# Kernel optimization log

Measured on AMD Instinct MI355X. Metric: run time of the kernel, lower is better.

## Reference

```python
import jax, jax.numpy as jnp
import numpy as np

N = 384       # nodes
K = 60        # neighbors per node
SUB = 20      # subsample_k
C_S = 128
C_Z = 128
H = 4
D_HEAD = C_Z // H
NUM_RBF = 64
E = N * K
EPS = 1e-8


def _rbf(D, D_min=0.0, D_max=20.0, D_count=NUM_RBF):
    # radial basis expansion of distances: [..., ] -> [..., D_count]
    mu = jnp.linspace(D_min, D_max, D_count)
    sigma = (D_max - D_min) / D_count
    return jnp.exp(-(((D[..., None] - mu) / sigma) ** 2))


def setup_inputs() -> dict:
    key = jax.random.key(0)
    ks = jax.random.split(key, 16)
    f32 = jnp.float32
    inp = {
        "node_features": jax.random.normal(ks[0], (N, C_S), f32),
        "node_trans": jax.random.normal(ks[1], (N, 3), f32) * 5.0,
        "edge_features": jax.random.normal(ks[2], (E, C_Z), f32),
        "edge_index": jax.random.randint(ks[3], (2, E), 0, N),
        "subsample_idx": jax.random.randint(ks[4], (N, K, SUB), 0, K),
        # dist_bias_gate: Linear(2*c_s -> H)
        "W_gate": jax.random.normal(ks[5], (2 * C_S, H), f32) / np.sqrt(2 * C_S),
        "b_gate": jnp.zeros((H,), f32),
        # dist_bias: Linear(num_rbf -> H)
        "W_db": jax.random.normal(ks[6], (NUM_RBF, H), f32) / np.sqrt(NUM_RBF),
        "b_db": jnp.zeros((H,), f32),
        # lin_qk: Linear(c_z -> 2*c_z)
        "W_qk": jax.random.normal(ks[7], (C_Z, 2 * C_Z), f32) / np.sqrt(C_Z),
        "b_qk": jnp.zeros((2 * C_Z,), f32),
        # lin_v: Linear(c_z -> c_z)
        "W_v": jax.random.normal(ks[8], (C_Z, C_Z), f32) / np.sqrt(C_Z),
        "b_v": jnp.zeros((C_Z,), f32),
        # lin_out: Linear(c_z -> c_z) (init='final' in source; random here for testing)
        "W_out": jax.random.normal(ks[9], (C_Z, C_Z), f32) / np.sqrt(C_Z),
        "b_out": jnp.zeros((C_Z,), f32),
    }
    return inp


def reference(node_features, node_trans, edge_features, edge_index, subsample_idx,
              W_gate, b_gate, W_db, b_db, W_qk, b_qk, W_v, b_v, W_out, b_out):
    n, k, sub = subsample_idx.shape
    # assume_sorted=True path: edges are grouped k-per-destination-node
    dst = edge_index[0].reshape(n, k)                           # [n,k] neighbor ids
    edge1 = jnp.broadcast_to(dst[:, :, None], (n, k, sub))      # [n,k,sub]
    edge2 = jnp.take_along_axis(
        jnp.broadcast_to(dst[:, None, :], (n, k, k)), subsample_idx, axis=-1)  # [n,k,sub]

    f1 = node_features[edge1]                                   # [n,k,sub,c_s]
    f2 = node_features[edge2]
    gate = jax.nn.sigmoid(jnp.concatenate([f1, f2], axis=-1) @ W_gate + b_gate)  # [n,k,sub,H]

    t1 = node_trans[edge1]                                      # [n,k,sub,3]
    t2 = node_trans[edge2]
    dist = jnp.linalg.norm(t1 - t2 + EPS, axis=-1)              # [n,k,sub]
    bias = gate * (_rbf(dist) @ W_db + b_db)                    # [n,k,sub,H]

    edges = edge_features.reshape(n, k, C_Z)
    qk = edges @ W_qk + b_qk
    q, kk = jnp.split(qk, 2, axis=-1)
    q = q.reshape(n, k, H, D_HEAD)
    kk = kk.reshape(n, k, H, D_HEAD)

    batch = jnp.arange(n)[:, None, None]
    k_sub = kk[batch, subsample_idx]                            # [n,k,sub,H,d]
    attn = jnp.einsum('nkhd,nkshd->nksh', q, k_sub) / np.sqrt(C_Z) + bias
    attn = jax.nn.softmax(attn, axis=2)                         # softmax over subsample axis

    v = (edges @ W_v + b_v).reshape(n, k, H, D_HEAD)
    v_sub = v[batch, subsample_idx]                             # [n,k,sub,H,d]
    upd = jnp.einsum('nksh,nkshd->nkhd', attn, v_sub).reshape(n * k, C_Z)
    return upd @ W_out + b_out                                  # [E, c_z]
```

## Files before the change

kernel.cpp:

```cpp
#include <hip/hip_runtime.h>
#include <hip/hip_bf16.h>

typedef unsigned short ushortT;
typedef __attribute__((ext_vector_type(8))) short bf16x8;
typedef __attribute__((ext_vector_type(4))) float f32x4;

#define N_NODES 384
#define KNBR 60
#define SUBK 20
#define NEDGE (N_NODES * KNBR)
#define EPSC 1e-8f
#define INV_SQRT_CZ 0.08838834764831845f
#define MU_STEP (20.0f / 63.0f)
#define INV_MU_STEP (63.0f / 20.0f)
#define INV_SIGMA 3.2f

__device__ __forceinline__ float bflo(unsigned int u) { return __uint_as_float(u << 16); }
__device__ __forceinline__ float bfhi(unsigned int u) { return __uint_as_float(u & 0xffff0000u); }
__device__ __forceinline__ ushortT f2bu(float v) {
  union { float f; unsigned int u; } c;
  c.f = v;
  return (ushortT)((c.u + 0x7fffu + ((c.u >> 16) & 1u)) >> 16);
}
__device__ __forceinline__ unsigned int pack2bf(float x, float y) {
  return (unsigned int)f2bu(x) | ((unsigned int)f2bu(y) << 16);
}
__device__ __forceinline__ ushortT f2h(float x) {
  _Float16 h = (_Float16)x;
  return __builtin_bit_cast(ushortT, h);
}
__device__ __forceinline__ float h2f(ushortT u) {
  return (float)__builtin_bit_cast(_Float16, u);
}

__global__ __launch_bounds__(256) void prep_kernel(
    const float* __restrict__ nf, const float* __restrict__ Wg, float* __restrict__ g,
    const float* __restrict__ Wqk, const float* __restrict__ bqk,
    const float* __restrict__ Wv, const float* __restrict__ bv,
    const float* __restrict__ Wout,
    ushortT* __restrict__ Wp1, ushortT* __restrict__ Wp2, float* __restrict__ bc) {
  int b = blockIdx.x, tid = threadIdx.x;
  if (b < 96) {
    int n = b * 4 + (tid >> 6), t = tid & 63;
    float a = nf[n * 128 + t];
    float bb = nf[n * 128 + 64 + t];
    float acc[8];
#pragma unroll
    for (int h = 0; h < 4; ++h) {
      acc[h]     = a * Wg[t * 4 + h]         + bb * Wg[(t + 64) * 4 + h];
      acc[4 + h] = a * Wg[(128 + t) * 4 + h] + bb * Wg[(192 + t) * 4 + h];
    }
#pragma unroll
    for (int i = 0; i < 8; ++i)
#pragma unroll
      for (int off = 32; off >= 1; off >>= 1) acc[i] += __shfl_xor(acc[i], off, 64);
    if (t == 0) {
#pragma unroll
      for (int i = 0; i < 8; ++i) g[n * 8 + i] = acc[i];
    }
  } else {
    int i = (b - 96) * 256 + tid;
    if (i < 49152) {
      int j = i & 7, l = (i >> 3) & 63, t = (i >> 9) & 3;
      int nt = (i >> 11) % 12, ny = (i >> 11) / 12;
      int nn = ny * 192 + nt * 16 + (l & 15);
      int k = t * 32 + (l >> 4) * 8 + j;
      float v = (nn < 256) ? Wqk[k * 256 + nn] : Wv[k * 128 + (nn - 256)];
      Wp1[i] = f2bu(v);
    } else {
      int i2 = i - 49152;
      int j = i2 & 7, l = (i2 >> 3) & 63, t = (i2 >> 9) & 3, nt = (i2 >> 11);
      int nn = nt * 16 + (l & 15);
      int k = t * 32 + (l >> 4) * 8 + j;
      Wp2[i2] = f2bu(Wout[k * 128 + nn]);
    }
    if (i < 384) bc[i] = (i < 256) ? bqk[i] : bv[i - 256];
  }
}

__global__ __launch_bounds__(512, 4) void fused_kernel(
    const float* __restrict__ ef, const ushortT* __restrict__ Wp1,
    const ushortT* __restrict__ Wp2, const float* __restrict__ bc,
    const float* __restrict__ bout, const float* __restrict__ g,
    const float* __restrict__ node_trans, const int* __restrict__ edge_index,
    const int* __restrict__ sub_idx, const float* __restrict__ W_db,
    const float* __restrict__ b_db, const float* __restrict__ b_gate,
    float* __restrict__ outp) {
  __shared__ __align__(16) ushortT kvb[KNBR * 256];
  __shared__ __align__(16) ushortT updq[64 * 136];
  __shared__ __align__(16) ushortT biasb[KNBR * SUBK * 4];
  __shared__ ushortT sub_lds[KNBR * SUBK];
  __shared__ float trs[KNBR * 3];
  __shared__ float gg[KNBR * 8];

  int n = blockIdx.x, tid = threadIdx.x;
  int e0 = n * KNBR;
  int w = tid >> 6, l = tid & 63;
  int lr = l & 15, lc = l >> 4;
  int rowA = (w & 3) * 16 + lr;
  int rowAc = min(rowA, KNBR - 1);

  if (tid < KNBR) {
    int dst = edge_index[e0 + tid];
#pragma unroll
    for (int c = 0; c < 3; ++c) trs[tid * 3 + c] = node_trans[dst * 3 + c];
#pragma unroll
    for (int i = 0; i < 8; ++i) gg[tid * 8 + i] = g[dst * 8 + i];
  }
  bf16x8 afrag[4];
#pragma unroll
  for (int t = 0; t < 4; ++t) {
    const float* ap = ef + (size_t)(e0 + rowAc) * 128 + t * 32 + lc * 8;
    float4 lo = *(const float4*)ap;
    float4 hi = *(const float4*)(ap + 4);
    bf16x8 a;
    a[0] = (short)f2bu(lo.x); a[1] = (short)f2bu(lo.y);
    a[2] = (short)f2bu(lo.z); a[3] = (short)f2bu(lo.w);
    a[4] = (short)f2bu(hi.x); a[5] = (short)f2bu(hi.y);
    a[6] = (short)f2bu(hi.z); a[7] = (short)f2bu(hi.w);
    afrag[t] = a;
  }

  int Tbase = (tid >> 8) * 12;
#pragma unroll
  for (int Ti = 0; Ti < 12; ++Ti) {
    int T = Tbase + Ti;
    f32x4 acc = {0.f, 0.f, 0.f, 0.f};
#pragma unroll
    for (int t = 0; t < 4; ++t) {
      bf16x8 bfrag = *(const bf16x8*)(Wp1 + ((T * 4 + t) * 64 + l) * 8);
      acc = __builtin_amdgcn_mfma_f32_16x16x32_bf16(bfrag, afrag[t], acc, 0, 0, 0);
    }
    int col0 = T * 16 + lc * 4;
    float4 bi = *(const float4*)(bc + col0);
    float o0 = acc[0] + bi.x, o1 = acc[1] + bi.y;
    float o2 = acc[2] + bi.z, o3 = acc[3] + bi.w;
    if (T < 8) {
      uint2 o;
      o.x = pack2bf(o0 * INV_SQRT_CZ, o1 * INV_SQRT_CZ);
      o.y = pack2bf(o2 * INV_SQRT_CZ, o3 * INV_SQRT_CZ);
      *(uint2*)(updq + rowA * 136 + col0) = o;
    } else if (rowA < KNBR) {
      uint2 o;
      o.x = pack2bf(o0, o1);
      o.y = pack2bf(o2, o3);
      int byteoff = ((col0 - 128) * 2) ^ ((rowA & 7) << 4);
      *(uint2*)((char*)kvb + rowA * 512 + byteoff) = o;
    }
  }
  __syncthreads();

  float4 bgv = *(const float4*)b_gate;
  float4 bdbv = *(const float4*)b_db;
  for (int p = tid; p < KNBR * SUBK; p += 512) {
    int kl = p / SUBK, s = p - kl * SUBK;
    int j = sub_idx[(size_t)(e0 + kl) * SUBK + s];
    sub_lds[p] = (ushortT)j;
    float dx = trs[kl * 3 + 0] - trs[j * 3 + 0] + EPSC;
    float dy = trs[kl * 3 + 1] - trs[j * 3 + 1] + EPSC;
    float dz = trs[kl * 3 + 2] - trs[j * 3 + 2] + EPSC;
    float dist = sqrtf(dx * dx + dy * dy + dz * dz);
    int r0 = (int)(dist * INV_MU_STEP + 0.5f);
    int rlo = max(r0 - 4, 0), rhi = min(r0 + 4, 63);
    float a0 = 0.f, a1 = 0.f, a2 = 0.f, a3 = 0.f;
    for (int r = rlo; r <= rhi; ++r) {
      float t = (dist - r * MU_STEP) * INV_SIGMA;
      float e = __expf(-t * t);
      float4 wv = ((const float4*)W_db)[r];
      a0 += e * wv.x; a1 += e * wv.y; a2 += e * wv.z; a3 += e * wv.w;
    }
    float g1 = gg[kl * 8 + 0] + gg[j * 8 + 4 + 0] + bgv.x;
    float g2 = gg[kl * 8 + 1] + gg[j * 8 + 4 + 1] + bgv.y;
    float g3 = gg[kl * 8 + 2] + gg[j * 8 + 4 + 2] + bgv.z;
    float g4 = gg[kl * 8 + 3] + gg[j * 8 + 4 + 3] + bgv.w;
    biasb[p * 4 + 0] = f2h((a0 + bdbv.x) / (1.0f + __expf(-g1)));
    biasb[p * 4 + 1] = f2h((a1 + bdbv.y) / (1.0f + __expf(-g2)));
    biasb[p * 4 + 2] = f2h((a2 + bdbv.z) / (1.0f + __expf(-g3)));
    biasb[p * 4 + 3] = f2h((a3 + bdbv.w) / (1.0f + __expf(-g4)));
  }
  __syncthreads();

  int row3 = tid >> 3, h = (tid >> 1) & 3, dh = tid & 1;
  int row3c = min(row3, KNBR - 1);
  const char* kvbase = (const char*)kvb;
  float qh[16];
  {
    const ushortT* qp = updq + row3 * 136 + h * 32 + dh * 16;
    uint4 u0 = *(const uint4*)qp;
    uint4 u1 = *(const uint4*)(qp + 8);
    qh[0] = bflo(u0.x); qh[1] = bfhi(u0.x); qh[2] = bflo(u0.y); qh[3] = bfhi(u0.y);
    qh[4] = bflo(u0.z); qh[5] = bfhi(u0.z); qh[6] = bflo(u0.w); qh[7] = bfhi(u0.w);
    qh[8] = bflo(u1.x); qh[9] = bfhi(u1.x); qh[10] = bflo(u1.y); qh[11] = bfhi(u1.y);
    qh[12] = bflo(u1.z); qh[13] = bfhi(u1.z); qh[14] = bflo(u1.w); qh[15] = bfhi(u1.w);
  }
  float logit[SUBK];
#pragma unroll
  for (int s = 0; s < SUBK; ++s) {
    int j = sub_lds[row3c * SUBK + s];
    int sw = (j & 7) << 4;
    float dot = 0.f;
#pragma unroll
    for (int c = 0; c < 2; ++c) {
      uint4 u = *(const uint4*)(kvbase + j * 512 + ((h * 64 + dh * 32 + c * 16) ^ sw));
      dot += qh[c * 8 + 0] * bflo(u.x) + qh[c * 8 + 1] * bfhi(u.x) +
             qh[c * 8 + 2] * bflo(u.y) + qh[c * 8 + 3] * bfhi(u.y) +
             qh[c * 8 + 4] * bflo(u.z) + qh[c * 8 + 5] * bfhi(u.z) +
             qh[c * 8 + 6] * bflo(u.w) + qh[c * 8 + 7] * bfhi(u.w);
    }
    dot += __shfl_xor(dot, 1);
    logit[s] = dot + h2f(biasb[(row3c * SUBK + s) * 4 + h]);
  }
  float m = logit[0];
#pragma unroll
  for (int s = 1; s < SUBK; ++s) m = fmaxf(m, logit[s]);
  float den = 0.f;
#pragma unroll
  for (int s = 0; s < SUBK; ++s) {
    logit[s] = __expf(logit[s] - m);
    den += logit[s];
  }
  float inv = 1.0f / den;
  float vacc[16];
#pragma unroll
  for (int i = 0; i < 16; ++i) vacc[i] = 0.f;
#pragma unroll
  for (int s = 0; s < SUBK; ++s) {
    int j = sub_lds[row3c * SUBK + s];
    int sw = (j & 7) << 4;
    float wgt = logit[s];
#pragma unroll
    for (int c = 0; c < 2; ++c) {
      uint4 u = *(const uint4*)(kvbase + j * 512 + ((256 + h * 64 + dh * 32 + c * 16) ^ sw));
      vacc[c * 8 + 0] += wgt * bflo(u.x); vacc[c * 8 + 1] += wgt * bfhi(u.x);
      vacc[c * 8 + 2] += wgt * bflo(u.y); vacc[c * 8 + 3] += wgt * bfhi(u.y);
      vacc[c * 8 + 4] += wgt * bflo(u.z); vacc[c * 8 + 5] += wgt * bfhi(u.z);
      vacc[c * 8 + 6] += wgt * bflo(u.w); vacc[c * 8 + 7] += wgt * bfhi(u.w);
    }
  }
#pragma unroll
  for (int c = 0; c < 2; ++c) {
    uint4 o;
    o.x = pack2bf(vacc[c * 8 + 0] * inv, vacc[c * 8 + 1] * inv);
    o.y = pack2bf(vacc[c * 8 + 2] * inv, vacc[c * 8 + 3] * inv);
    o.z = pack2bf(vacc[c * 8 + 4] * inv, vacc[c * 8 + 5] * inv);
    o.w = pack2bf(vacc[c * 8 + 6] * inv, vacc[c * 8 + 7] * inv);
    *(uint4*)(updq + row3 * 136 + h * 32 + dh * 16 + c * 8) = o;
  }
  __syncthreads();

  bf16x8 af2[4];
#pragma unroll
  for (int t = 0; t < 4; ++t)
    af2[t] = *(const bf16x8*)(updq + rowA * 136 + t * 32 + lc * 8);
  int T4base = (tid >> 8) * 4;
#pragma unroll
  for (int Ti = 0; Ti < 4; ++Ti) {
    int T = T4base + Ti;
    f32x4 acc = {0.f, 0.f, 0.f, 0.f};
#pragma unroll
    for (int t = 0; t < 4; ++t) {
      bf16x8 bfrag = *(const bf16x8*)(Wp2 + ((T * 4 + t) * 64 + l) * 8);
      acc = __builtin_amdgcn_mfma_f32_16x16x32_bf16(bfrag, af2[t], acc, 0, 0, 0);
    }
    if (rowA < KNBR) {
      int col0 = T * 16 + lc * 4;
      float4 bi = *(const float4*)(bout + col0);
      float4 o;
      o.x = acc[0] + bi.x; o.y = acc[1] + bi.y;
      o.z = acc[2] + bi.z; o.w = acc[3] + bi.w;
      *(float4*)(outp + (size_t)(e0 + rowA) * 128 + col0) = o;
    }
  }
}

extern "C" void kernel_launch(void* const* d_in, const int* in_sizes, int n_in, void* d_out,
                              int out_size, void* d_ws, size_t ws_size, hipStream_t stream) {
  const float* nf  = (const float*)d_in[0];
  const float* nt  = (const float*)d_in[1];
  const float* ef  = (const float*)d_in[2];
  const int*   ei  = (const int*)d_in[3];
  const int*   si  = (const int*)d_in[4];
  const float* Wg  = (const float*)d_in[5];
  const float* bg  = (const float*)d_in[6];
  const float* Wdb = (const float*)d_in[7];
  const float* bdb = (const float*)d_in[8];
  const float* Wqk = (const float*)d_in[9];
  const float* bqk = (const float*)d_in[10];
  const float* Wv  = (const float*)d_in[11];
  const float* bv  = (const float*)d_in[12];
  const float* Wout = (const float*)d_in[13];
  const float* bout = (const float*)d_in[14];
  float* out = (float*)d_out;

  float* g      = (float*)d_ws;
  float* bc     = g + 3072;
  ushortT* Wp1  = (ushortT*)(bc + 384);
  ushortT* Wp2  = Wp1 + 49152;

  prep_kernel<<<dim3(352), dim3(256), 0, stream>>>(nf, Wg, g, Wqk, bqk, Wv, bv, Wout,
                                                   Wp1, Wp2, bc);
  fused_kernel<<<dim3(N_NODES), dim3(512), 0, stream>>>(ef, Wp1, Wp2, bc, bout, g, nt, ei, si,
                                                        Wdb, bdb, bg, out);
}
```

Measured before the change: 40.20 us.

## Split each node's edge rows across two 256-thread blocks

Launches a 384x2 grid of 256-thread blocks, each handling 30 of the 60 edge rows for Q, bias, attention and output. Every block still computes the full K/V projection for all 60 neighbours, since subsampled keys can come from either half. The K/V LDS layout is also re-swizzled so each thread's head slice sits in 16-byte chunks. The aim is more blocks and better CU fill, at the cost of doing the K/V GEMM and the ef loads twice.

```diff
diff --git a/kernel.cpp b/kernel.cpp
--- a/kernel.cpp
+++ b/kernel.cpp
@@ -14,6 +14,7 @@
 #define MU_STEP (20.0f / 63.0f)
 #define INV_MU_STEP (63.0f / 20.0f)
 #define INV_SIGMA 3.2f
+#define RHALF 30
 
 __device__ __forceinline__ float bflo(unsigned int u) { return __uint_as_float(u << 16); }
 __device__ __forceinline__ float bfhi(unsigned int u) { return __uint_as_float(u & 0xffff0000u); }
@@ -78,7 +79,7 @@
   }
 }
 
-__global__ __launch_bounds__(512, 4) void fused_kernel(
+__global__ __launch_bounds__(256, 3) void fused_kernel(
     const float* __restrict__ ef, const ushortT* __restrict__ Wp1,
     const ushortT* __restrict__ Wp2, const float* __restrict__ bc,
     const float* __restrict__ bout, const float* __restrict__ g,
@@ -87,18 +88,15 @@
     const float* __restrict__ b_db, const float* __restrict__ b_gate,
     float* __restrict__ outp) {
   __shared__ __align__(16) ushortT kvb[KNBR * 256];
-  __shared__ __align__(16) ushortT updq[64 * 136];
-  __shared__ __align__(16) ushortT biasb[KNBR * SUBK * 4];
-  __shared__ ushortT sub_lds[KNBR * SUBK];
+  __shared__ __align__(16) ushortT updq[32 * 136];
+  __shared__ __align__(16) ushortT biasb[RHALF * SUBK * 4];
+  __shared__ ushortT sub_lds[RHALF * SUBK];
   __shared__ float trs[KNBR * 3];
   __shared__ float gg[KNBR * 8];
 
-  int n = blockIdx.x, tid = threadIdx.x;
-  int e0 = n * KNBR;
-  int w = tid >> 6, l = tid & 63;
-  int lr = l & 15, lc = l >> 4;
-  int rowA = (w & 3) * 16 + lr;
-  int rowAc = min(rowA, KNBR - 1);
+  int n = blockIdx.x, half = blockIdx.y, tid = threadIdx.x;
+  int e0 = n * KNBR, r0 = half * RHALF;
+  int w = tid >> 6, l = tid & 63, lr = l & 15, lc = l >> 4;
 
   if (tid < KNBR) {
     int dst = edge_index[e0 + tid];
@@ -107,10 +105,15 @@
 #pragma unroll
     for (int i = 0; i < 8; ++i) gg[tid * 8 + i] = g[dst * 8 + i];
   }
-  bf16x8 afrag[4];
+  int kvrow = w * 16 + lr;
+  int kvrowc = min(kvrow, KNBR - 1);
+  int qlrow = (w & 1) * 16 + lr;
+  int qrowg = r0 + min(qlrow, RHALF - 1);
+
+  bf16x8 afKV[4], afQ[4];
 #pragma unroll
   for (int t = 0; t < 4; ++t) {
-    const float* ap = ef + (size_t)(e0 + rowAc) * 128 + t * 32 + lc * 8;
+    const float* ap = ef + (size_t)(e0 + kvrowc) * 128 + t * 32 + lc * 8;
     float4 lo = *(const float4*)ap;
     float4 hi = *(const float4*)(ap + 4);
     bf16x8 a;
@@ -118,50 +121,71 @@
     a[2] = (short)f2bu(lo.z); a[3] = (short)f2bu(lo.w);
     a[4] = (short)f2bu(hi.x); a[5] = (short)f2bu(hi.y);
     a[6] = (short)f2bu(hi.z); a[7] = (short)f2bu(hi.w);
-    afrag[t] = a;
-  }
-
-  int Tbase = (tid >> 8) * 12;
-#pragma unroll
-  for (int Ti = 0; Ti < 12; ++Ti) {
-    int T = Tbase + Ti;
+    afKV[t] = a;
+    const float* aq = ef + (size_t)(e0 + qrowg) * 128 + t * 32 + lc * 8;
+    float4 lo2 = *(const float4*)aq;
+    float4 hi2 = *(const float4*)(aq + 4);
+    bf16x8 b;
+    b[0] = (short)f2bu(lo2.x); b[1] = (short)f2bu(lo2.y);
+    b[2] = (short)f2bu(lo2.z); b[3] = (short)f2bu(lo2.w);
+    b[4] = (short)f2bu(hi2.x); b[5] = (short)f2bu(hi2.y);
+    b[6] = (short)f2bu(hi2.z); b[7] = (short)f2bu(hi2.w);
+    afQ[t] = b;
+  }
+
+#pragma unroll
+  for (int Ti = 0; Ti < 4; ++Ti) {
+    int T = (w >> 1) * 4 + Ti;
     f32x4 acc = {0.f, 0.f, 0.f, 0.f};
 #pragma unroll
     for (int t = 0; t < 4; ++t) {
       bf16x8 bfrag = *(const bf16x8*)(Wp1 + ((T * 4 + t) * 64 + l) * 8);
-      acc = __builtin_amdgcn_mfma_f32_16x16x32_bf16(bfrag, afrag[t], acc, 0, 0, 0);
+      acc = __builtin_amdgcn_mfma_f32_16x16x32_bf16(bfrag, afQ[t], acc, 0, 0, 0);
     }
     int col0 = T * 16 + lc * 4;
     float4 bi = *(const float4*)(bc + col0);
-    float o0 = acc[0] + bi.x, o1 = acc[1] + bi.y;
-    float o2 = acc[2] + bi.z, o3 = acc[3] + bi.w;
-    if (T < 8) {
+    uint2 o;
+    o.x = pack2bf((acc[0] + bi.x) * INV_SQRT_CZ, (acc[1] + bi.y) * INV_SQRT_CZ);
+    o.y = pack2bf((acc[2] + bi.z) * INV_SQRT_CZ, (acc[3] + bi.w) * INV_SQRT_CZ);
+    *(uint2*)(updq + qlrow * 136 + col0) = o;
+  }
+#pragma unroll
+  for (int Ti = 0; Ti < 16; ++Ti) {
+    int T = 8 + Ti;
+    f32x4 acc = {0.f, 0.f, 0.f, 0.f};
+#pragma unroll
+    for (int t = 0; t < 4; ++t) {
+      bf16x8 bfrag = *(const bf16x8*)(Wp1 + ((T * 4 + t) * 64 + l) * 8);
+      acc = __builtin_amdgcn_mfma_f32_16x16x32_bf16(bfrag, afKV[t], acc, 0, 0, 0);
+    }
+    int col0 = T * 16 + lc * 4;
+    float4 bi = *(const float4*)(bc + col0);
+    if (kvrow < KNBR) {
       uint2 o;
-      o.x = pack2bf(o0 * INV_SQRT_CZ, o1 * INV_SQRT_CZ);
-      o.y = pack2bf(o2 * INV_SQRT_CZ, o3 * INV_SQRT_CZ);
-      *(uint2*)(updq + rowA * 136 + col0) = o;
-    } else if (rowA < KNBR) {
-      uint2 o;
-      o.x = pack2bf(o0, o1);
-      o.y = pack2bf(o2, o3);
-      int byteoff = ((col0 - 128) * 2) ^ ((rowA & 7) << 4);
-      *(uint2*)((char*)kvb + rowA * 512 + byteoff) = o;
+      o.x = pack2bf(acc[0] + bi.x, acc[1] + bi.y);
+      o.y = pack2bf(acc[2] + bi.z, acc[3] + bi.w);
+      int colk = col0 - 128;
+      int base_b = (colk & 128) << 1;
+      int d = colk & 127;
+      int inner = (((d >> 3) & 1) * 128 + (d >> 4) * 16 + (d & 7) * 2) ^ ((kvrow & 7) << 4);
+      *(uint2*)((char*)kvb + kvrow * 512 + base_b + inner) = o;
     }
   }
   __syncthreads();
 
   float4 bgv = *(const float4*)b_gate;
   float4 bdbv = *(const float4*)b_db;
-  for (int p = tid; p < KNBR * SUBK; p += 512) {
+  for (int p = tid; p < RHALF * SUBK; p += 256) {
     int kl = p / SUBK, s = p - kl * SUBK;
-    int j = sub_idx[(size_t)(e0 + kl) * SUBK + s];
+    int kg = r0 + kl;
+    int j = sub_idx[(size_t)(e0 + kg) * SUBK + s];
     sub_lds[p] = (ushortT)j;
-    float dx = trs[kl * 3 + 0] - trs[j * 3 + 0] + EPSC;
-    float dy = trs[kl * 3 + 1] - trs[j * 3 + 1] + EPSC;
-    float dz = trs[kl * 3 + 2] - trs[j * 3 + 2] + EPSC;
+    float dx = trs[kg * 3 + 0] - trs[j * 3 + 0] + EPSC;
+    float dy = trs[kg * 3 + 1] - trs[j * 3 + 1] + EPSC;
+    float dz = trs[kg * 3 + 2] - trs[j * 3 + 2] + EPSC;
     float dist = sqrtf(dx * dx + dy * dy + dz * dz);
-    int r0 = (int)(dist * INV_MU_STEP + 0.5f);
-    int rlo = max(r0 - 4, 0), rhi = min(r0 + 4, 63);
+    int r00 = (int)(dist * INV_MU_STEP + 0.5f);
+    int rlo = max(r00 - 4, 0), rhi = min(r00 + 4, 63);
     float a0 = 0.f, a1 = 0.f, a2 = 0.f, a3 = 0.f;
     for (int r = rlo; r <= rhi; ++r) {
       float t = (dist - r * MU_STEP) * INV_SIGMA;
@@ -169,10 +193,10 @@
       float4 wv = ((const float4*)W_db)[r];
       a0 += e * wv.x; a1 += e * wv.y; a2 += e * wv.z; a3 += e * wv.w;
     }
-    float g1 = gg[kl * 8 + 0] + gg[j * 8 + 4 + 0] + bgv.x;
-    float g2 = gg[kl * 8 + 1] + gg[j * 8 + 4 + 1] + bgv.y;
-    float g3 = gg[kl * 8 + 2] + gg[j * 8 + 4 + 2] + bgv.z;
-    float g4 = gg[kl * 8 + 3] + gg[j * 8 + 4 + 3] + bgv.w;
+    float g1 = gg[kg * 8 + 0] + gg[j * 8 + 4 + 0] + bgv.x;
+    float g2 = gg[kg * 8 + 1] + gg[j * 8 + 4 + 1] + bgv.y;
+    float g3 = gg[kg * 8 + 2] + gg[j * 8 + 4 + 2] + bgv.z;
+    float g4 = gg[kg * 8 + 3] + gg[j * 8 + 4 + 3] + bgv.w;
     biasb[p * 4 + 0] = f2h((a0 + bdbv.x) / (1.0f + __expf(-g1)));
     biasb[p * 4 + 1] = f2h((a1 + bdbv.y) / (1.0f + __expf(-g2)));
     biasb[p * 4 + 2] = f2h((a2 + bdbv.z) / (1.0f + __expf(-g3)));
@@ -180,95 +204,99 @@
   }
   __syncthreads();
 
-  int row3 = tid >> 3, h = (tid >> 1) & 3, dh = tid & 1;
-  int row3c = min(row3, KNBR - 1);
-  const char* kvbase = (const char*)kvb;
-  float qh[16];
-  {
-    const ushortT* qp = updq + row3 * 136 + h * 32 + dh * 16;
-    uint4 u0 = *(const uint4*)qp;
-    uint4 u1 = *(const uint4*)(qp + 8);
-    qh[0] = bflo(u0.x); qh[1] = bfhi(u0.x); qh[2] = bflo(u0.y); qh[3] = bfhi(u0.y);
-    qh[4] = bflo(u0.z); qh[5] = bfhi(u0.z); qh[6] = bflo(u0.w); qh[7] = bfhi(u0.w);
-    qh[8] = bflo(u1.x); qh[9] = bfhi(u1.x); qh[10] = bflo(u1.y); qh[11] = bfhi(u1.y);
-    qh[12] = bflo(u1.z); qh[13] = bfhi(u1.z); qh[14] = bflo(u1.w); qh[15] = bfhi(u1.w);
-  }
-  float logit[SUBK];
-#pragma unroll
-  for (int s = 0; s < SUBK; ++s) {
-    int j = sub_lds[row3c * SUBK + s];
-    int sw = (j & 7) << 4;
-    float dot = 0.f;
+  int row3 = tid >> 3;
+  if (row3 < RHALF) {
+    int h = (tid >> 1) & 3, dh = tid & 1;
+    int hd = h * 2 + dh;
+    const char* kvbase = (const char*)kvb;
+    float qh[16];
+    {
+      const ushortT* qp = updq + row3 * 136 + h * 32 + dh * 16;
+      uint4 u0 = *(const uint4*)qp;
+      uint4 u1 = *(const uint4*)(qp + 8);
+      qh[0] = bflo(u0.x); qh[1] = bfhi(u0.x); qh[2] = bflo(u0.y); qh[3] = bfhi(u0.y);
+      qh[4] = bflo(u0.z); qh[5] = bfhi(u0.z); qh[6] = bflo(u0.w); qh[7] = bfhi(u0.w);
+      qh[8] = bflo(u1.x); qh[9] = bfhi(u1.x); qh[10] = bflo(u1.y); qh[11] = bfhi(u1.y);
+      qh[12] = bflo(u1.z); qh[13] = bfhi(u1.z); qh[14] = bflo(u1.w); qh[15] = bfhi(u1.w);
+    }
+    float logit[SUBK];
+#pragma unroll
+    for (int s = 0; s < SUBK; ++s) {
+      int j = sub_lds[row3 * SUBK + s];
+      int sw = (j & 7) << 4;
+      float dot = 0.f;
+#pragma unroll
+      for (int c = 0; c < 2; ++c) {
+        uint4 u = *(const uint4*)(kvbase + j * 512 + ((c * 128 + hd * 16) ^ sw));
+        dot += qh[c * 8 + 0] * bflo(u.x) + qh[c * 8 + 1] * bfhi(u.x) +
+               qh[c * 8 + 2] * bflo(u.y) + qh[c * 8 + 3] * bfhi(u.y) +
+               qh[c * 8 + 4] * bflo(u.z) + qh[c * 8 + 5] * bfhi(u.z) +
+               qh[c * 8 + 6] * bflo(u.w) + qh[c * 8 + 7] * bfhi(u.w);
+      }
+      dot += __shfl_xor(dot, 1);
+      logit[s] = dot + h2f(biasb[(row3 * SUBK + s) * 4 + h]);
+    }
+    float m = logit[0];
+#pragma unroll
+    for (int s = 1; s < SUBK; ++s) m = fmaxf(m, logit[s]);
+    float den = 0.f;
+#pragma unroll
+    for (int s = 0; s < SUBK; ++s) {
+      logit[s] = __expf(logit[s] - m);
+      den += logit[s];
+    }
+    float inv = 1.0f / den;
+    float vacc[16];
+#pragma unroll
+    for (int i = 0; i < 16; ++i) vacc[i] = 0.f;
+#pragma unroll
+    for (int s = 0; s < SUBK; ++s) {
+      int j = sub_lds[row3 * SUBK + s];
+      int sw = (j & 7) << 4;
+      float wgt = logit[s];
+#pragma unroll
+      for (int c = 0; c < 2; ++c) {
+        uint4 u = *(const uint4*)(kvbase + j * 512 + 256 + ((c * 128 + hd * 16) ^ sw));
+        vacc[c * 8 + 0] += wgt * bflo(u.x); vacc[c * 8 + 1] += wgt * bfhi(u.x);
+        vacc[c * 8 + 2] += wgt * bflo(u.y); vacc[c * 8 + 3] += wgt * bfhi(u.y);
+        vacc[c * 8 + 4] += wgt * bflo(u.z); vacc[c * 8 + 5] += wgt * bfhi(u.z);
+        vacc[c * 8 + 6] += wgt * bflo(u.w); vacc[c * 8 + 7] += wgt * bfhi(u.w);
+      }
+    }
 #pragma unroll
     for (int c = 0; c < 2; ++c) {
-      uint4 u = *(const uint4*)(kvbase + j * 512 + ((h * 64 + dh * 32 + c * 16) ^ sw));
-      dot += qh[c * 8 + 0] * bflo(u.x) + qh[c * 8 + 1] * bfhi(u.x) +
-             qh[c * 8 + 2] * bflo(u.y) + qh[c * 8 + 3] * bfhi(u.y) +
-             qh[c * 8 + 4] * bflo(u.z) + qh[c * 8 + 5] * bfhi(u.z) +
-             qh[c * 8 + 6] * bflo(u.w) + qh[c * 8 + 7] * bfhi(u.w);
-    }
-    dot += __shfl_xor(dot, 1);
-    logit[s] = dot + h2f(biasb[(row3c * SUBK + s) * 4 + h]);
-  }
-  float m = logit[0];
-#pragma unroll
-  for (int s = 1; s < SUBK; ++s) m = fmaxf(m, logit[s]);
-  float den = 0.f;
-#pragma unroll
-  for (int s = 0; s < SUBK; ++s) {
-    logit[s] = __expf(logit[s] - m);
-    den += logit[s];
-  }
-  float inv = 1.0f / den;
-  float vacc[16];
-#pragma unroll
-  for (int i = 0; i < 16; ++i) vacc[i] = 0.f;
-#pragma unroll
-  for (int s = 0; s < SUBK; ++s) {
-    int j = sub_lds[row3c * SUBK + s];
-    int sw = (j & 7) << 4;
-    float wgt = logit[s];
-#pragma unroll
-    for (int c = 0; c < 2; ++c) {
-      uint4 u = *(const uint4*)(kvbase + j * 512 + ((256 + h * 64 + dh * 32 + c * 16) ^ sw));
-      vacc[c * 8 + 0] += wgt * bflo(u.x); vacc[c * 8 + 1] += wgt * bfhi(u.x);
-      vacc[c * 8 + 2] += wgt * bflo(u.y); vacc[c * 8 + 3] += wgt * bfhi(u.y);
-      vacc[c * 8 + 4] += wgt * bflo(u.z); vacc[c * 8 + 5] += wgt * bfhi(u.z);
-      vacc[c * 8 + 6] += wgt * bflo(u.w); vacc[c * 8 + 7] += wgt * bfhi(u.w);
-    }
-  }
-#pragma unroll
-  for (int c = 0; c < 2; ++c) {
-    uint4 o;
-    o.x = pack2bf(vacc[c * 8 + 0] * inv, vacc[c * 8 + 1] * inv);
-    o.y = pack2bf(vacc[c * 8 + 2] * inv, vacc[c * 8 + 3] * inv);
-    o.z = pack2bf(vacc[c * 8 + 4] * inv, vacc[c * 8 + 5] * inv);
-    o.w = pack2bf(vacc[c * 8 + 6] * inv, vacc[c * 8 + 7] * inv);
-    *(uint4*)(updq + row3 * 136 + h * 32 + dh * 16 + c * 8) = o;
+      uint4 o;
+      o.x = pack2bf(vacc[c * 8 + 0] * inv, vacc[c * 8 + 1] * inv);
+      o.y = pack2bf(vacc[c * 8 + 2] * inv, vacc[c * 8 + 3] * inv);
+      o.z = pack2bf(vacc[c * 8 + 4] * inv, vacc[c * 8 + 5] * inv);
+      o.w = pack2bf(vacc[c * 8 + 6] * inv, vacc[c * 8 + 7] * inv);
+      *(uint4*)(updq + row3 * 136 + h * 32 + dh * 16 + c * 8) = o;
+    }
   }
   __syncthreads();
 
+  int lrow = (w & 1) * 16 + lr;
+  int lrowc = min(lrow, RHALF - 1);
   bf16x8 af2[4];
 #pragma unroll
   for (int t = 0; t < 4; ++t)
-    af2[t] = *(const bf16x8*)(updq + rowA * 136 + t * 32 + lc * 8);
-  int T4base = (tid >> 8) * 4;
+    af2[t] = *(const bf16x8*)(updq + lrowc * 136 + t * 32 + lc * 8);
 #pragma unroll
   for (int Ti = 0; Ti < 4; ++Ti) {
-    int T = T4base + Ti;
+    int T = (w >> 1) * 4 + Ti;
     f32x4 acc = {0.f, 0.f, 0.f, 0.f};
 #pragma unroll
     for (int t = 0; t < 4; ++t) {
       bf16x8 bfrag = *(const bf16x8*)(Wp2 + ((T * 4 + t) * 64 + l) * 8);
       acc = __builtin_amdgcn_mfma_f32_16x16x32_bf16(bfrag, af2[t], acc, 0, 0, 0);
     }
-    if (rowA < KNBR) {
+    if (lrow < RHALF) {
       int col0 = T * 16 + lc * 4;
       float4 bi = *(const float4*)(bout + col0);
       float4 o;
       o.x = acc[0] + bi.x; o.y = acc[1] + bi.y;
       o.z = acc[2] + bi.z; o.w = acc[3] + bi.w;
-      *(float4*)(outp + (size_t)(e0 + rowA) * 128 + col0) = o;
+      *(float4*)(outp + (size_t)(e0 + r0 + lrow) * 128 + col0) = o;
     }
   }
 }
@@ -299,6 +327,6 @@
 
   prep_kernel<<<dim3(352), dim3(256), 0, stream>>>(nf, Wg, g, Wqk, bqk, Wv, bv, Wout,
                                                    Wp1, Wp2, bc);
-  fused_kernel<<<dim3(N_NODES), dim3(512), 0, stream>>>(ef, Wp1, Wp2, bc, bout, g, nt, ei, si,
-                                                        Wdb, bdb, bg, out);
-}
+  fused_kernel<<<dim3(N_NODES, 2), dim3(256), 0, stream>>>(ef, Wp1, Wp2, bc, bout, g, nt,
+                                                           ei, si, Wdb, bdb, bg, out);
+}
```

Measured after the change: 93.10 us. +131.6%, slower.
